# Performance work log

Measured on AMD Instinct MI355X. Metric: run time of the kernel, lower is better.

The kernel has to match this reference:

```python
import jax, jax.numpy as jnp
import numpy as np

N_POINTS = 200000   # number of voxels
N_CLUSTS = 4096     # number of clusters
P = 64              # points per cluster (regularized fixed size)
E = 32768           # number of (directed) edges


def setup_inputs() -> dict:
    key = jax.random.key(0)
    k1, k2, k3 = jax.random.split(key, 3)
    data = jax.random.normal(k1, (N_POINTS, 4), dtype=jnp.float32)
    clusts = jax.random.randint(k2, (N_CLUSTS, P), 0, N_POINTS, dtype=jnp.int64)
    edge_index = jax.random.randint(k3, (2, E), 0, N_CLUSTS, dtype=jnp.int64)
    return {"data": data, "clusts": clusts, "edge_index": edge_index}


def reference(data, clusts, edge_index):
    coords = data[:, 1:4]                      # [N, 3] voxel coordinates
    c1 = clusts[edge_index[0]]                 # [E, P] point indices of source cluster
    c2 = clusts[edge_index[1]]                 # [E, P] point indices of target cluster
    x1 = coords[c1]                            # [E, P, 3]
    x2 = coords[c2]                            # [E, P, 3]
    e, p = c1.shape
    # pairwise squared distances per edge: [E, P, P]
    d2 = jnp.sum((x1[:, :, None, :] - x2[:, None, :, :]) ** 2, axis=-1)
    imin = jnp.argmin(d2.reshape(e, p * p), axis=1)   # flat argmin of closest pair
    i1 = imin // p
    i2 = imin % p
    v1 = jnp.take_along_axis(x1, i1[:, None, None], axis=1)[:, 0, :]  # [E, 3]
    v2 = jnp.take_along_axis(x2, i2[:, None, None], axis=1)[:, 0, :]  # [E, 3]
    disp = v1 - v2                                                    # [E, 3]
    lend = jnp.linalg.norm(disp, axis=1, keepdims=True)               # [E, 1]
    safe = jnp.where(lend > 0, lend, jnp.ones_like(lend))
    disp = jnp.where(lend > 0, disp / safe, disp)                     # unit displacement
    B = (disp[:, :, None] * disp[:, None, :]).reshape(e, 9)           # outer product, flat
    return jnp.concatenate([v1, v2, disp, lend, B], axis=1)           # [E, 19]
```

## Files before the change

### kernel.cpp

```cpp
#include <hip/hip_runtime.h>

#ifndef FLT_MAX
#define FLT_MAX 3.402823466e+38f
#endif

typedef float v2f __attribute__((ext_vector_type(2)));
typedef float v4f __attribute__((ext_vector_type(4)));

__device__ __forceinline__ float sel3(int i, float a, float b, float c) {
    return i == 0 ? a : (i == 1 ? b : c);
}

__device__ __forceinline__ float sel4(int i, float a, float b, float c, float d) {
    return i == 0 ? a : (i == 1 ? b : (i == 2 ? c : d));
}

__device__ __forceinline__ float d2f(float ax, float ay, float az,
                                     float bx, float by, float bz) {
    const float dx = __fsub_rn(ax, bx);
    const float dy = __fsub_rn(ay, by);
    const float dz = __fsub_rn(az, bz);
    return __builtin_fmaf(dx, dx, __builtin_fmaf(dy, dy, __fmul_rn(dz, dz)));
}

__device__ __forceinline__ v2f d2p(v2f ax, v2f ay, v2f az, v2f bx, v2f by, v2f bz) {
    const v2f dx = ax - bx, dy = ay - by, dz = az - bz;
    return __builtin_elementwise_fma(dx, dx,
           __builtin_elementwise_fma(dy, dy, dz * dz));
}

#define SLICE 196

__global__ __launch_bounds__(256, 4) void clustgeo_edge_kernel(
    const float* __restrict__ data,
    const int*   __restrict__ clusts,
    const int*   __restrict__ eidx,
    float*       __restrict__ out,
    int E)
{
    const int wave = threadIdx.x >> 6;
    const int lane = threadIdx.x & 63;
    const int t    = lane & 15;
    const int gsh  = lane & 48;
    const int e    = blockIdx.x * 16 + wave * 4 + (lane >> 4);
    const int ec   = e < E ? e : (E - 1);

    __shared__ __align__(16) float sx[4][4][SLICE];

    const int ca = eidx[ec];
    const int cb = eidx[E + ec];

    const int4 P1 = *reinterpret_cast<const int4*>(clusts + ca * 64 + 4 * t);
    const int4 P2 = *reinterpret_cast<const int4*>(clusts + cb * 64 + 4 * t);
    const float4 q10 = *reinterpret_cast<const float4*>(data + (size_t)P1.x * 4);
    const float4 q11 = *reinterpret_cast<const float4*>(data + (size_t)P1.y * 4);
    const float4 q12 = *reinterpret_cast<const float4*>(data + (size_t)P1.z * 4);
    const float4 q13 = *reinterpret_cast<const float4*>(data + (size_t)P1.w * 4);
    const float4 q20 = *reinterpret_cast<const float4*>(data + (size_t)P2.x * 4);
    const float4 q21 = *reinterpret_cast<const float4*>(data + (size_t)P2.y * 4);
    const float4 q22 = *reinterpret_cast<const float4*>(data + (size_t)P2.z * 4);
    const float4 q23 = *reinterpret_cast<const float4*>(data + (size_t)P2.w * 4);
    const float r0x=q10.y, r0y=q10.z, r0z=q10.w;
    const float r1x=q11.y, r1y=q11.z, r1z=q11.w;
    const float r2x=q12.y, r2y=q12.z, r2z=q12.w;
    const float r3x=q13.y, r3y=q13.z, r3z=q13.w;
    const float c0x=q20.y, c0y=q20.z, c0z=q20.w;
    const float c1x=q21.y, c1y=q21.z, c1z=q21.w;
    const float c2x=q22.y, c2y=q22.z, c2z=q22.w;
    const float c3x=q23.y, c3y=q23.z, c3z=q23.w;

    float* slice = &sx[wave][lane >> 4][0];
    *reinterpret_cast<v4f*>(slice + 4 * t)       = (v4f){c0x, c1x, c2x, c3x};
    *reinterpret_cast<v4f*>(slice + 64 + 4 * t)  = (v4f){c0y, c1y, c2y, c3y};
    *reinterpret_cast<v4f*>(slice + 128 + 4 * t) = (v4f){c0z, c1z, c2z, c3z};

    const v4f* SL = reinterpret_cast<const v4f*>(slice);

    v2f a0 = {FLT_MAX, FLT_MAX}, a1 = {FLT_MAX, FLT_MAX};
    v2f a2 = {FLT_MAX, FLT_MAX}, a3 = {FLT_MAX, FLT_MAX};
    #pragma unroll 2
    for (int g = 0; g < 16; ++g) {
        const v4f X = SL[g];
        const v4f Y = SL[16 + g];
        const v4f Z = SL[32 + g];
        const v2f xlo = X.xy, xhi = X.zw, ylo = Y.xy, yhi = Y.zw, zlo = Z.xy, zhi = Z.zw;
        a0 = __builtin_elementwise_min(a0, d2p((v2f){r0x,r0x},(v2f){r0y,r0y},(v2f){r0z,r0z}, xlo, ylo, zlo));
        a0 = __builtin_elementwise_min(a0, d2p((v2f){r0x,r0x},(v2f){r0y,r0y},(v2f){r0z,r0z}, xhi, yhi, zhi));
        a1 = __builtin_elementwise_min(a1, d2p((v2f){r1x,r1x},(v2f){r1y,r1y},(v2f){r1z,r1z}, xlo, ylo, zlo));
        a1 = __builtin_elementwise_min(a1, d2p((v2f){r1x,r1x},(v2f){r1y,r1y},(v2f){r1z,r1z}, xhi, yhi, zhi));
        a2 = __builtin_elementwise_min(a2, d2p((v2f){r2x,r2x},(v2f){r2y,r2y},(v2f){r2z,r2z}, xlo, ylo, zlo));
        a2 = __builtin_elementwise_min(a2, d2p((v2f){r2x,r2x},(v2f){r2y,r2y},(v2f){r2z,r2z}, xhi, yhi, zhi));
        a3 = __builtin_elementwise_min(a3, d2p((v2f){r3x,r3x},(v2f){r3y,r3y},(v2f){r3z,r3z}, xlo, ylo, zlo));
        a3 = __builtin_elementwise_min(a3, d2p((v2f){r3x,r3x},(v2f){r3y,r3y},(v2f){r3z,r3z}, xhi, yhi, zhi));
    }
    const float m0 = fminf(a0.x, a0.y);
    const float m1 = fminf(a1.x, a1.y);
    const float m2 = fminf(a2.x, a2.y);
    const float m3 = fminf(a3.x, a3.y);

    float bmn = fminf(fminf(m0, m1), fminf(m2, m3));
    #pragma unroll
    for (int off = 8; off; off >>= 1) bmn = fminf(bmn, __shfl_xor(bmn, off, 64));

    const unsigned g0 = (unsigned)(__ballot(m0 == bmn) >> gsh) & 0xFFFFu;
    const unsigned g1 = (unsigned)(__ballot(m1 == bmn) >> gsh) & 0xFFFFu;
    const unsigned g2 = (unsigned)(__ballot(m2 == bmn) >> gsh) & 0xFFFFu;
    const unsigned g3 = (unsigned)(__ballot(m3 == bmn) >> gsh) & 0xFFFFu;
    const int t1 = __builtin_ctz(g0 | g1 | g2 | g3);
    const int s1 = (g0 >> t1) & 1 ? 0 : (g1 >> t1) & 1 ? 1 : (g2 >> t1) & 1 ? 2 : 3;

    const float v1x = __shfl(sel4(s1, r0x, r1x, r2x, r3x), gsh + t1, 64);
    const float v1y = __shfl(sel4(s1, r0y, r1y, r2y, r3y), gsh + t1, 64);
    const float v1z = __shfl(sel4(s1, r0z, r1z, r2z, r3z), gsh + t1, 64);

    const float d0 = d2f(v1x, v1y, v1z, c0x, c0y, c0z);
    const float d1 = d2f(v1x, v1y, v1z, c1x, c1y, c1z);
    const float d2_ = d2f(v1x, v1y, v1z, c2x, c2y, c2z);
    const float d3 = d2f(v1x, v1y, v1z, c3x, c3y, c3z);
    const unsigned h0 = (unsigned)(__ballot(d0 == bmn) >> gsh) & 0xFFFFu;
    const unsigned h1 = (unsigned)(__ballot(d1 == bmn) >> gsh) & 0xFFFFu;
    const unsigned h2 = (unsigned)(__ballot(d2_ == bmn) >> gsh) & 0xFFFFu;
    const unsigned h3 = (unsigned)(__ballot(d3 == bmn) >> gsh) & 0xFFFFu;
    const int t2 = __builtin_ctz(h0 | h1 | h2 | h3);
    const int s2 = (h0 >> t2) & 1 ? 0 : (h1 >> t2) & 1 ? 1 : (h2 >> t2) & 1 ? 2 : 3;

    const float v2x = __shfl(sel4(s2, c0x, c1x, c2x, c3x), gsh + t2, 64);
    const float v2y = __shfl(sel4(s2, c0y, c1y, c2y, c3y), gsh + t2, 64);
    const float v2z = __shfl(sel4(s2, c0z, c1z, c2z, c3z), gsh + t2, 64);

    float dx = v1x - v2x, dy = v1y - v2y, dz = v1z - v2z;
    const float lend = sqrtf(dx * dx + dy * dy + dz * dz);
    if (lend > 0.f) { dx /= lend; dy /= lend; dz /= lend; }

    if (e < E) {
        float* orow = out + (size_t)e * 19;
        float o;
        if (t < 3)       o = sel3(t,     v1x, v1y, v1z);
        else if (t < 6)  o = sel3(t - 3, v2x, v2y, v2z);
        else if (t < 9)  o = sel3(t - 6, dx, dy, dz);
        else if (t == 9) o = lend;
        else {
            const int k = t - 10;
            o = sel3(k / 3, dx, dy, dz) * sel3(k % 3, dx, dy, dz);
        }
        orow[t] = o;
        if (t < 3) {
            const int k = t + 6;
            orow[16 + t] = sel3(k / 3, dx, dy, dz) * sel3(k % 3, dx, dy, dz);
        }
    }
}

extern "C" void kernel_launch(void* const* d_in, const int* in_sizes, int n_in,
                              void* d_out, int out_size, void* d_ws, size_t ws_size,
                              hipStream_t stream) {
    const float* data   = (const float*)d_in[0];
    const int*   clusts = (const int*)d_in[1];
    const int*   eidx   = (const int*)d_in[2];
    float*       out    = (float*)d_out;
    const int E = in_sizes[2] / 2;
    const int blocks = (E + 15) / 16;
    clustgeo_edge_kernel<<<blocks, 256, 0, stream>>>(data, clusts, eidx, out, E);
}
```

Measured before the change: 31.87 us.

## Pre-gather cluster coordinates into SoA table before per-edge scan

Adds a pre-pass kernel that gathers each cluster's 64 point coordinates into a contiguous SoA table (x, y, z rows) in workspace. The per-edge kernel then reads coalesced float4 vectors from this table instead of doing a double indirection through clusts and scattered 16-byte loads from data for every edge. This avoids re-gathering the same cluster points about 16 times across edges, at the cost of an extra kernel launch and a round trip to the table (about 3 MB). If the workspace is too small, it falls back to the original single kernel.

Result: slower. 35.45 us (+11.2%).

```diff
diff --git a/kernel.cpp b/kernel.cpp
--- a/kernel.cpp
+++ b/kernel.cpp
@@ -29,11 +29,27 @@
            __builtin_elementwise_fma(dy, dy, dz * dz));
 }
 
-#define SLICE 196
-
-__global__ __launch_bounds__(256, 4) void clustgeo_edge_kernel(
+__global__ __launch_bounds__(256) void build_table_kernel(
     const float* __restrict__ data,
     const int*   __restrict__ clusts,
+    float*       __restrict__ T,
+    int C)
+{
+    const int c = blockIdx.x * 4 + (threadIdx.x >> 6);
+    const int p = threadIdx.x & 63;
+    if (c >= C) return;
+    const int pid = clusts[c * 64 + p];
+    const float4 d = *reinterpret_cast<const float4*>(data + (size_t)pid * 4);
+    float* row = T + (size_t)c * 192;
+    row[p]       = d.y;
+    row[p + 64]  = d.z;
+    row[p + 128] = d.w;
+}
+
+#define SLICE 196
+
+__global__ __launch_bounds__(256, 4) void clustgeo_scan_kernel(
+    const float* __restrict__ T,
     const int*   __restrict__ eidx,
     float*       __restrict__ out,
     int E)
@@ -49,30 +65,24 @@
 
     const int ca = eidx[ec];
     const int cb = eidx[E + ec];
-
-    const int4 P1 = *reinterpret_cast<const int4*>(clusts + ca * 64 + 4 * t);
-    const int4 P2 = *reinterpret_cast<const int4*>(clusts + cb * 64 + 4 * t);
-    const float4 q10 = *reinterpret_cast<const float4*>(data + (size_t)P1.x * 4);
-    const float4 q11 = *reinterpret_cast<const float4*>(data + (size_t)P1.y * 4);
-    const float4 q12 = *reinterpret_cast<const float4*>(data + (size_t)P1.z * 4);
-    const float4 q13 = *reinterpret_cast<const float4*>(data + (size_t)P1.w * 4);
-    const float4 q20 = *reinterpret_cast<const float4*>(data + (size_t)P2.x * 4);
-    const float4 q21 = *reinterpret_cast<const float4*>(data + (size_t)P2.y * 4);
-    const float4 q22 = *reinterpret_cast<const float4*>(data + (size_t)P2.z * 4);
-    const float4 q23 = *reinterpret_cast<const float4*>(data + (size_t)P2.w * 4);
-    const float r0x=q10.y, r0y=q10.z, r0z=q10.w;
-    const float r1x=q11.y, r1y=q11.z, r1z=q11.w;
-    const float r2x=q12.y, r2y=q12.z, r2z=q12.w;
-    const float r3x=q13.y, r3y=q13.z, r3z=q13.w;
-    const float c0x=q20.y, c0y=q20.z, c0z=q20.w;
-    const float c1x=q21.y, c1y=q21.z, c1z=q21.w;
-    const float c2x=q22.y, c2y=q22.z, c2z=q22.w;
-    const float c3x=q23.y, c3y=q23.z, c3z=q23.w;
+    const float* Ta = T + (size_t)ca * 192;
+    const float* Tb = T + (size_t)cb * 192;
+
+    const v4f RX = *reinterpret_cast<const v4f*>(Ta + 4 * t);
+    const v4f RY = *reinterpret_cast<const v4f*>(Ta + 64 + 4 * t);
+    const v4f RZ = *reinterpret_cast<const v4f*>(Ta + 128 + 4 * t);
+    const v4f CX = *reinterpret_cast<const v4f*>(Tb + 4 * t);
+    const v4f CY = *reinterpret_cast<const v4f*>(Tb + 64 + 4 * t);
+    const v4f CZ = *reinterpret_cast<const v4f*>(Tb + 128 + 4 * t);
 
     float* slice = &sx[wave][lane >> 4][0];
-    *reinterpret_cast<v4f*>(slice + 4 * t)       = (v4f){c0x, c1x, c2x, c3x};
-    *reinterpret_cast<v4f*>(slice + 64 + 4 * t)  = (v4f){c0y, c1y, c2y, c3y};
-    *reinterpret_cast<v4f*>(slice + 128 + 4 * t) = (v4f){c0z, c1z, c2z, c3z};
+    *reinterpret_cast<v4f*>(slice + 4 * t)       = CX;
+    *reinterpret_cast<v4f*>(slice + 64 + 4 * t)  = CY;
+    *reinterpret_cast<v4f*>(slice + 128 + 4 * t) = CZ;
+
+    const float r0x=RX.x, r1x=RX.y, r2x=RX.z, r3x=RX.w;
+    const float r0y=RY.x, r1y=RY.y, r2y=RY.z, r3y=RY.w;
+    const float r0z=RZ.x, r1z=RZ.y, r2z=RZ.z, r3z=RZ.w;
 
     const v4f* SL = reinterpret_cast<const v4f*>(slice);
 
@@ -109,14 +119,14 @@
     const int t1 = __builtin_ctz(g0 | g1 | g2 | g3);
     const int s1 = (g0 >> t1) & 1 ? 0 : (g1 >> t1) & 1 ? 1 : (g2 >> t1) & 1 ? 2 : 3;
 
-    const float v1x = __shfl(sel4(s1, r0x, r1x, r2x, r3x), gsh + t1, 64);
-    const float v1y = __shfl(sel4(s1, r0y, r1y, r2y, r3y), gsh + t1, 64);
-    const float v1z = __shfl(sel4(s1, r0z, r1z, r2z, r3z), gsh + t1, 64);
-
-    const float d0 = d2f(v1x, v1y, v1z, c0x, c0y, c0z);
-    const float d1 = d2f(v1x, v1y, v1z, c1x, c1y, c1z);
-    const float d2_ = d2f(v1x, v1y, v1z, c2x, c2y, c2z);
-    const float d3 = d2f(v1x, v1y, v1z, c3x, c3y, c3z);
+    const float v1x = __shfl(sel4(s1, RX.x, RX.y, RX.z, RX.w), gsh + t1, 64);
+    const float v1y = __shfl(sel4(s1, RY.x, RY.y, RY.z, RY.w), gsh + t1, 64);
+    const float v1z = __shfl(sel4(s1, RZ.x, RZ.y, RZ.z, RZ.w), gsh + t1, 64);
+
+    const float d0 = d2f(v1x, v1y, v1z, CX.x, CY.x, CZ.x);
+    const float d1 = d2f(v1x, v1y, v1z, CX.y, CY.y, CZ.y);
+    const float d2_ = d2f(v1x, v1y, v1z, CX.z, CY.z, CZ.z);
+    const float d3 = d2f(v1x, v1y, v1z, CX.w, CY.w, CZ.w);
     const unsigned h0 = (unsigned)(__ballot(d0 == bmn) >> gsh) & 0xFFFFu;
     const unsigned h1 = (unsigned)(__ballot(d1 == bmn) >> gsh) & 0xFFFFu;
     const unsigned h2 = (unsigned)(__ballot(d2_ == bmn) >> gsh) & 0xFFFFu;
@@ -124,9 +134,9 @@
     const int t2 = __builtin_ctz(h0 | h1 | h2 | h3);
     const int s2 = (h0 >> t2) & 1 ? 0 : (h1 >> t2) & 1 ? 1 : (h2 >> t2) & 1 ? 2 : 3;
 
-    const float v2x = __shfl(sel4(s2, c0x, c1x, c2x, c3x), gsh + t2, 64);
-    const float v2y = __shfl(sel4(s2, c0y, c1y, c2y, c3y), gsh + t2, 64);
-    const float v2z = __shfl(sel4(s2, c0z, c1z, c2z, c3z), gsh + t2, 64);
+    const float v2x = __shfl(sel4(s2, CX.x, CX.y, CX.z, CX.w), gsh + t2, 64);
+    const float v2y = __shfl(sel4(s2, CY.x, CY.y, CY.z, CY.w), gsh + t2, 64);
+    const float v2z = __shfl(sel4(s2, CZ.x, CZ.y, CZ.z, CZ.w), gsh + t2, 64);
 
     float dx = v1x - v2x, dy = v1y - v2y, dz = v1z - v2z;
     const float lend = sqrtf(dx * dx + dy * dy + dz * dz);
@@ -151,6 +161,115 @@
     }
 }
 
+__global__ __launch_bounds__(256, 4) void clustgeo_edge_fallback(
+    const float* __restrict__ data,
+    const int*   __restrict__ clusts,
+    const int*   __restrict__ eidx,
+    float*       __restrict__ out,
+    int E)
+{
+    const int wave = threadIdx.x >> 6;
+    const int lane = threadIdx.x & 63;
+    const int t    = lane & 15;
+    const int gsh  = lane & 48;
+    const int e    = blockIdx.x * 16 + wave * 4 + (lane >> 4);
+    const int ec   = e < E ? e : (E - 1);
+
+    __shared__ __align__(16) float sx[4][4][SLICE];
+
+    const int ca = eidx[ec];
+    const int cb = eidx[E + ec];
+    const int4 P1 = *reinterpret_cast<const int4*>(clusts + ca * 64 + 4 * t);
+    const int4 P2 = *reinterpret_cast<const int4*>(clusts + cb * 64 + 4 * t);
+    const float4 q10 = *reinterpret_cast<const float4*>(data + (size_t)P1.x * 4);
+    const float4 q11 = *reinterpret_cast<const float4*>(data + (size_t)P1.y * 4);
+    const float4 q12 = *reinterpret_cast<const float4*>(data + (size_t)P1.z * 4);
+    const float4 q13 = *reinterpret_cast<const float4*>(data + (size_t)P1.w * 4);
+    const float4 q20 = *reinterpret_cast<const float4*>(data + (size_t)P2.x * 4);
+    const float4 q21 = *reinterpret_cast<const float4*>(data + (size_t)P2.y * 4);
+    const float4 q22 = *reinterpret_cast<const float4*>(data + (size_t)P2.z * 4);
+    const float4 q23 = *reinterpret_cast<const float4*>(data + (size_t)P2.w * 4);
+    const v4f RX = {q10.y, q11.y, q12.y, q13.y};
+    const v4f RY = {q10.z, q11.z, q12.z, q13.z};
+    const v4f RZ = {q10.w, q11.w, q12.w, q13.w};
+    const v4f CX = {q20.y, q21.y, q22.y, q23.y};
+    const v4f CY = {q20.z, q21.z, q22.z, q23.z};
+    const v4f CZ = {q20.w, q21.w, q22.w, q23.w};
+
+    float* slice = &sx[wave][lane >> 4][0];
+    *reinterpret_cast<v4f*>(slice + 4 * t)       = CX;
+    *reinterpret_cast<v4f*>(slice + 64 + 4 * t)  = CY;
+    *reinterpret_cast<v4f*>(slice + 128 + 4 * t) = CZ;
+
+    const v4f* SL = reinterpret_cast<const v4f*>(slice);
+    v2f a0 = {FLT_MAX, FLT_MAX}, a1 = {FLT_MAX, FLT_MAX};
+    v2f a2 = {FLT_MAX, FLT_MAX}, a3 = {FLT_MAX, FLT_MAX};
+    #pragma unroll 2
+    for (int g = 0; g < 16; ++g) {
+        const v4f X = SL[g];
+        const v4f Y = SL[16 + g];
+        const v4f Z = SL[32 + g];
+        const v2f xlo = X.xy, xhi = X.zw, ylo = Y.xy, yhi = Y.zw, zlo = Z.xy, zhi = Z.zw;
+        a0 = __builtin_elementwise_min(a0, d2p((v2f){RX.x,RX.x},(v2f){RY.x,RY.x},(v2f){RZ.x,RZ.x}, xlo, ylo, zlo));
+        a0 = __builtin_elementwise_min(a0, d2p((v2f){RX.x,RX.x},(v2f){RY.x,RY.x},(v2f){RZ.x,RZ.x}, xhi, yhi, zhi));
+        a1 = __builtin_elementwise_min(a1, d2p((v2f){RX.y,RX.y},(v2f){RY.y,RY.y},(v2f){RZ.y,RZ.y}, xlo, ylo, zlo));
+        a1 = __builtin_elementwise_min(a1, d2p((v2f){RX.y,RX.y},(v2f){RY.y,RY.y},(v2f){RZ.y,RZ.y}, xhi, yhi, zhi));
+        a2 = __builtin_elementwise_min(a2, d2p((v2f){RX.z,RX.z},(v2f){RY.z,RY.z},(v2f){RZ.z,RZ.z}, xlo, ylo, zlo));
+        a2 = __builtin_elementwise_min(a2, d2p((v2f){RX.z,RX.z},(v2f){RY.z,RY.z},(v2f){RZ.z,RZ.z}, xhi, yhi, zhi));
+        a3 = __builtin_elementwise_min(a3, d2p((v2f){RX.w,RX.w},(v2f){RY.w,RY.w},(v2f){RZ.w,RZ.w}, xlo, ylo, zlo));
+        a3 = __builtin_elementwise_min(a3, d2p((v2f){RX.w,RX.w},(v2f){RY.w,RY.w},(v2f){RZ.w,RZ.w}, xhi, yhi, zhi));
+    }
+    const float m0 = fminf(a0.x, a0.y);
+    const float m1 = fminf(a1.x, a1.y);
+    const float m2 = fminf(a2.x, a2.y);
+    const float m3 = fminf(a3.x, a3.y);
+    float bmn = fminf(fminf(m0, m1), fminf(m2, m3));
+    #pragma unroll
+    for (int off = 8; off; off >>= 1) bmn = fminf(bmn, __shfl_xor(bmn, off, 64));
+    const unsigned g0 = (unsigned)(__ballot(m0 == bmn) >> gsh) & 0xFFFFu;
+    const unsigned g1 = (unsigned)(__ballot(m1 == bmn) >> gsh) & 0xFFFFu;
+    const unsigned g2 = (unsigned)(__ballot(m2 == bmn) >> gsh) & 0xFFFFu;
+    const unsigned g3 = (unsigned)(__ballot(m3 == bmn) >> gsh) & 0xFFFFu;
+    const int t1 = __builtin_ctz(g0 | g1 | g2 | g3);
+    const int s1 = (g0 >> t1) & 1 ? 0 : (g1 >> t1) & 1 ? 1 : (g2 >> t1) & 1 ? 2 : 3;
+    const float v1x = __shfl(sel4(s1, RX.x, RX.y, RX.z, RX.w), gsh + t1, 64);
+    const float v1y = __shfl(sel4(s1, RY.x, RY.y, RY.z, RY.w), gsh + t1, 64);
+    const float v1z = __shfl(sel4(s1, RZ.x, RZ.y, RZ.z, RZ.w), gsh + t1, 64);
+    const float d0 = d2f(v1x, v1y, v1z, CX.x, CY.x, CZ.x);
+    const float d1 = d2f(v1x, v1y, v1z, CX.y, CY.y, CZ.y);
+    const float d2_ = d2f(v1x, v1y, v1z, CX.z, CY.z, CZ.z);
+    const float d3 = d2f(v1x, v1y, v1z, CX.w, CY.w, CZ.w);
+    const unsigned h0 = (unsigned)(__ballot(d0 == bmn) >> gsh) & 0xFFFFu;
+    const unsigned h1 = (unsigned)(__ballot(d1 == bmn) >> gsh) & 0xFFFFu;
+    const unsigned h2 = (unsigned)(__ballot(d2_ == bmn) >> gsh) & 0xFFFFu;
+    const unsigned h3 = (unsigned)(__ballot(d3 == bmn) >> gsh) & 0xFFFFu;
+    const int t2 = __builtin_ctz(h0 | h1 | h2 | h3);
+    const int s2 = (h0 >> t2) & 1 ? 0 : (h1 >> t2) & 1 ? 1 : (h2 >> t2) & 1 ? 2 : 3;
+    const float v2x = __shfl(sel4(s2, CX.x, CX.y, CX.z, CX.w), gsh + t2, 64);
+    const float v2y = __shfl(sel4(s2, CY.x, CY.y, CY.z, CY.w), gsh + t2, 64);
+    const float v2z = __shfl(sel4(s2, CZ.x, CZ.y, CZ.z, CZ.w), gsh + t2, 64);
+    float dx = v1x - v2x, dy = v1y - v2y, dz = v1z - v2z;
+    const float lend = sqrtf(dx * dx + dy * dy + dz * dz);
+    if (lend > 0.f) { dx /= lend; dy /= lend; dz /= lend; }
+    if (e < E) {
+        float* orow = out + (size_t)e * 19;
+        float o;
+        if (t < 3)       o = sel3(t,     v1x, v1y, v1z);
+        else if (t < 6)  o = sel3(t - 3, v2x, v2y, v2z);
+        else if (t < 9)  o = sel3(t - 6, dx, dy, dz);
+        else if (t == 9) o = lend;
+        else {
+            const int k = t - 10;
+            o = sel3(k / 3, dx, dy, dz) * sel3(k % 3, dx, dy, dz);
+        }
+        orow[t] = o;
+        if (t < 3) {
+            const int k = t + 6;
+            orow[16 + t] = sel3(k / 3, dx, dy, dz) * sel3(k % 3, dx, dy, dz);
+        }
+    }
+}
+
 extern "C" void kernel_launch(void* const* d_in, const int* in_sizes, int n_in,
                               void* d_out, int out_size, void* d_ws, size_t ws_size,
                               hipStream_t stream) {
@@ -159,6 +278,14 @@
     const int*   eidx   = (const int*)d_in[2];
     float*       out    = (float*)d_out;
     const int E = in_sizes[2] / 2;
-    const int blocks = (E + 15) / 16;
-    clustgeo_edge_kernel<<<blocks, 256, 0, stream>>>(data, clusts, eidx, out, E);
-}
+    const int C = in_sizes[1] / 64;
+    const size_t tbytes = (size_t)C * 192 * sizeof(float);
+
+    if (ws_size >= tbytes) {
+        float* T = (float*)d_ws;
+        build_table_kernel<<<(C + 3) / 4, 256, 0, stream>>>(data, clusts, T, C);
+        clustgeo_scan_kernel<<<(E + 15) / 16, 256, 0, stream>>>(T, eidx, out, E);
+    } else {
+        clustgeo_edge_fallback<<<(E + 15) / 16, 256, 0, stream>>>(data, clusts, eidx, out, E);
+    }
+}
```

## Filter closest-pair candidates with packed fp16 distances, refine rows exactly in fp32

Applied to the files above, without the earlier changes.

The 64x64 pairwise distance scan now runs in packed fp16 (v_pk_add/fma/min via inline asm) on negated, fp16-packed target coordinates held in LDS, with half the LDS footprint. Rows whose fp16 minimum falls within an error bound of the best are kept as candidates. Each candidate row is then recomputed exactly in fp32, one row at a time across the 16-lane group, to recover the true argmin. This halves the work of the main loop but adds a serial refinement loop whose trip count depends on the data, and it relies on a heuristic error bound that could miss the true minimum or overflow fp16 for large coordinates.

Result: slower. 60.75 us (+90.6%).

```diff
diff --git a/kernel.cpp b/kernel.cpp
--- a/kernel.cpp
+++ b/kernel.cpp
@@ -4,34 +4,50 @@
 #define FLT_MAX 3.402823466e+38f
 #endif
 
-typedef float v2f __attribute__((ext_vector_type(2)));
-typedef float v4f __attribute__((ext_vector_type(4)));
-
 __device__ __forceinline__ float sel3(int i, float a, float b, float c) {
     return i == 0 ? a : (i == 1 ? b : c);
 }
-
 __device__ __forceinline__ float sel4(int i, float a, float b, float c, float d) {
     return i == 0 ? a : (i == 1 ? b : (i == 2 ? c : d));
 }
 
-__device__ __forceinline__ float d2f(float ax, float ay, float az,
-                                     float bx, float by, float bz) {
+__device__ __forceinline__ float d2np(float ax, float ay, float az,
+                                      float bx, float by, float bz) {
     const float dx = __fsub_rn(ax, bx);
     const float dy = __fsub_rn(ay, by);
     const float dz = __fsub_rn(az, bz);
-    return __builtin_fmaf(dx, dx, __builtin_fmaf(dy, dy, __fmul_rn(dz, dz)));
-}
-
-__device__ __forceinline__ v2f d2p(v2f ax, v2f ay, v2f az, v2f bx, v2f by, v2f bz) {
-    const v2f dx = ax - bx, dy = ay - by, dz = az - bz;
-    return __builtin_elementwise_fma(dx, dx,
-           __builtin_elementwise_fma(dy, dy, dz * dz));
-}
-
-#define SLICE 196
-
-__global__ __launch_bounds__(256, 4) void clustgeo_edge_kernel(
+    return __fadd_rn(__fadd_rn(__fmul_rn(dx, dx), __fmul_rn(dy, dy)),
+                     __fmul_rn(dz, dz));
+}
+
+__device__ __forceinline__ unsigned pk2(float a, float b) {
+    unsigned short ua = __builtin_bit_cast(unsigned short, (_Float16)a);
+    unsigned short ub = __builtin_bit_cast(unsigned short, (_Float16)b);
+    return (unsigned)ua | ((unsigned)ub << 16);
+}
+__device__ __forceinline__ float lo16f(unsigned u) {
+    return (float)__builtin_bit_cast(_Float16, (unsigned short)(u & 0xFFFFu));
+}
+__device__ __forceinline__ float hi16f(unsigned u) {
+    return (float)__builtin_bit_cast(_Float16, (unsigned short)(u >> 16));
+}
+
+__device__ __forceinline__ void f16step(unsigned& acc, unsigned rx, unsigned ry,
+                                        unsigned rz, unsigned ncx, unsigned ncy,
+                                        unsigned ncz) {
+    unsigned dx, dy, dz;
+    asm("v_pk_add_f16 %0, %4, %7\n\t"
+        "v_pk_add_f16 %1, %5, %8\n\t"
+        "v_pk_add_f16 %2, %6, %9\n\t"
+        "v_pk_mul_f16 %2, %2, %2\n\t"
+        "v_pk_fma_f16 %2, %1, %1, %2\n\t"
+        "v_pk_fma_f16 %2, %0, %0, %2\n\t"
+        "v_pk_min_f16 %3, %3, %2"
+        : "=&v"(dx), "=&v"(dy), "=&v"(dz), "+v"(acc)
+        : "v"(rx), "v"(ry), "v"(rz), "v"(ncx), "v"(ncy), "v"(ncz));
+}
+
+__global__ __launch_bounds__(256, 4) void clustgeo_f16filter(
     const float* __restrict__ data,
     const int*   __restrict__ clusts,
     const int*   __restrict__ eidx,
@@ -45,11 +61,10 @@
     const int e    = blockIdx.x * 16 + wave * 4 + (lane >> 4);
     const int ec   = e < E ? e : (E - 1);
 
-    __shared__ __align__(16) float sx[4][4][SLICE];
+    __shared__ __align__(16) unsigned sx[4][4][112];
 
     const int ca = eidx[ec];
     const int cb = eidx[E + ec];
-
     const int4 P1 = *reinterpret_cast<const int4*>(clusts + ca * 64 + 4 * t);
     const int4 P2 = *reinterpret_cast<const int4*>(clusts + cb * 64 + 4 * t);
     const float4 q10 = *reinterpret_cast<const float4*>(data + (size_t)P1.x * 4);
@@ -69,68 +84,121 @@
     const float c2x=q22.y, c2y=q22.z, c2z=q22.w;
     const float c3x=q23.y, c3y=q23.z, c3z=q23.w;
 
-    float* slice = &sx[wave][lane >> 4][0];
-    *reinterpret_cast<v4f*>(slice + 4 * t)       = (v4f){c0x, c1x, c2x, c3x};
-    *reinterpret_cast<v4f*>(slice + 64 + 4 * t)  = (v4f){c0y, c1y, c2y, c3y};
-    *reinterpret_cast<v4f*>(slice + 128 + 4 * t) = (v4f){c0z, c1z, c2z, c3z};
-
-    const v4f* SL = reinterpret_cast<const v4f*>(slice);
-
-    v2f a0 = {FLT_MAX, FLT_MAX}, a1 = {FLT_MAX, FLT_MAX};
-    v2f a2 = {FLT_MAX, FLT_MAX}, a3 = {FLT_MAX, FLT_MAX};
+    unsigned* slice = &sx[wave][lane >> 4][0];
+    slice[2*t]        = pk2(-c0x, -c1x);  slice[2*t + 1]      = pk2(-c2x, -c3x);
+    slice[32 + 2*t]   = pk2(-c0y, -c1y);  slice[32 + 2*t + 1] = pk2(-c2y, -c3y);
+    slice[64 + 2*t]   = pk2(-c0z, -c1z);  slice[64 + 2*t + 1] = pk2(-c2z, -c3z);
+
+    const unsigned rr0x = pk2(r0x, r0x), rr0y = pk2(r0y, r0y), rr0z = pk2(r0z, r0z);
+    const unsigned rr1x = pk2(r1x, r1x), rr1y = pk2(r1y, r1y), rr1z = pk2(r1z, r1z);
+    const unsigned rr2x = pk2(r2x, r2x), rr2y = pk2(r2y, r2y), rr2z = pk2(r2z, r2z);
+    const unsigned rr3x = pk2(r3x, r3x), rr3y = pk2(r3y, r3y), rr3z = pk2(r3z, r3z);
+
+    const uint4* SU = reinterpret_cast<const uint4*>(slice);
+    unsigned a0 = 0x7C007C00u, a1 = 0x7C007C00u;
+    unsigned a2 = 0x7C007C00u, a3 = 0x7C007C00u;
+
     #pragma unroll 2
-    for (int g = 0; g < 16; ++g) {
-        const v4f X = SL[g];
-        const v4f Y = SL[16 + g];
-        const v4f Z = SL[32 + g];
-        const v2f xlo = X.xy, xhi = X.zw, ylo = Y.xy, yhi = Y.zw, zlo = Z.xy, zhi = Z.zw;
-        a0 = __builtin_elementwise_min(a0, d2p((v2f){r0x,r0x},(v2f){r0y,r0y},(v2f){r0z,r0z}, xlo, ylo, zlo));
-        a0 = __builtin_elementwise_min(a0, d2p((v2f){r0x,r0x},(v2f){r0y,r0y},(v2f){r0z,r0z}, xhi, yhi, zhi));
-        a1 = __builtin_elementwise_min(a1, d2p((v2f){r1x,r1x},(v2f){r1y,r1y},(v2f){r1z,r1z}, xlo, ylo, zlo));
-        a1 = __builtin_elementwise_min(a1, d2p((v2f){r1x,r1x},(v2f){r1y,r1y},(v2f){r1z,r1z}, xhi, yhi, zhi));
-        a2 = __builtin_elementwise_min(a2, d2p((v2f){r2x,r2x},(v2f){r2y,r2y},(v2f){r2z,r2z}, xlo, ylo, zlo));
-        a2 = __builtin_elementwise_min(a2, d2p((v2f){r2x,r2x},(v2f){r2y,r2y},(v2f){r2z,r2z}, xhi, yhi, zhi));
-        a3 = __builtin_elementwise_min(a3, d2p((v2f){r3x,r3x},(v2f){r3y,r3y},(v2f){r3z,r3z}, xlo, ylo, zlo));
-        a3 = __builtin_elementwise_min(a3, d2p((v2f){r3x,r3x},(v2f){r3y,r3y},(v2f){r3z,r3z}, xhi, yhi, zhi));
-    }
-    const float m0 = fminf(a0.x, a0.y);
-    const float m1 = fminf(a1.x, a1.y);
-    const float m2 = fminf(a2.x, a2.y);
-    const float m3 = fminf(a3.x, a3.y);
-
-    float bmn = fminf(fminf(m0, m1), fminf(m2, m3));
+    for (int g = 0; g < 8; ++g) {
+        const uint4 X = SU[g];
+        const uint4 Y = SU[8 + g];
+        const uint4 Z = SU[16 + g];
+        f16step(a0, rr0x, rr0y, rr0z, X.x, Y.x, Z.x);
+        f16step(a0, rr0x, rr0y, rr0z, X.y, Y.y, Z.y);
+        f16step(a0, rr0x, rr0y, rr0z, X.z, Y.z, Z.z);
+        f16step(a0, rr0x, rr0y, rr0z, X.w, Y.w, Z.w);
+        f16step(a1, rr1x, rr1y, rr1z, X.x, Y.x, Z.x);
+        f16step(a1, rr1x, rr1y, rr1z, X.y, Y.y, Z.y);
+        f16step(a1, rr1x, rr1y, rr1z, X.z, Y.z, Z.z);
+        f16step(a1, rr1x, rr1y, rr1z, X.w, Y.w, Z.w);
+        f16step(a2, rr2x, rr2y, rr2z, X.x, Y.x, Z.x);
+        f16step(a2, rr2x, rr2y, rr2z, X.y, Y.y, Z.y);
+        f16step(a2, rr2x, rr2y, rr2z, X.z, Y.z, Z.z);
+        f16step(a2, rr2x, rr2y, rr2z, X.w, Y.w, Z.w);
+        f16step(a3, rr3x, rr3y, rr3z, X.x, Y.x, Z.x);
+        f16step(a3, rr3x, rr3y, rr3z, X.y, Y.y, Z.y);
+        f16step(a3, rr3x, rr3y, rr3z, X.z, Y.z, Z.z);
+        f16step(a3, rr3x, rr3y, rr3z, X.w, Y.w, Z.w);
+    }
+
+    const float rm0 = fminf(lo16f(a0), hi16f(a0));
+    const float rm1 = fminf(lo16f(a1), hi16f(a1));
+    const float rm2 = fminf(lo16f(a2), hi16f(a2));
+    const float rm3 = fminf(lo16f(a3), hi16f(a3));
+
+    float bm = fminf(fminf(rm0, rm1), fminf(rm2, rm3));
     #pragma unroll
-    for (int off = 8; off; off >>= 1) bmn = fminf(bmn, __shfl_xor(bmn, off, 64));
-
-    const unsigned g0 = (unsigned)(__ballot(m0 == bmn) >> gsh) & 0xFFFFu;
-    const unsigned g1 = (unsigned)(__ballot(m1 == bmn) >> gsh) & 0xFFFFu;
-    const unsigned g2 = (unsigned)(__ballot(m2 == bmn) >> gsh) & 0xFFFFu;
-    const unsigned g3 = (unsigned)(__ballot(m3 == bmn) >> gsh) & 0xFFFFu;
-    const int t1 = __builtin_ctz(g0 | g1 | g2 | g3);
-    const int s1 = (g0 >> t1) & 1 ? 0 : (g1 >> t1) & 1 ? 1 : (g2 >> t1) & 1 ? 2 : 3;
-
+    for (int off = 8; off; off >>= 1) bm = fminf(bm, __shfl_xor(bm, off, 64));
+
+    float Ml = fmaxf(fmaxf(fmaxf(fabsf(r0x), fabsf(r0y)), fmaxf(fabsf(r0z), fabsf(r1x))),
+               fmaxf(fmaxf(fabsf(r1y), fabsf(r1z)), fmaxf(fabsf(r2x), fabsf(r2y))));
+    Ml = fmaxf(Ml, fmaxf(fmaxf(fabsf(r2z), fabsf(r3x)), fmaxf(fabsf(r3y), fabsf(r3z))));
+    Ml = fmaxf(Ml, fmaxf(fmaxf(fabsf(c0x), fabsf(c0y)), fmaxf(fabsf(c0z), fabsf(c1x))));
+    Ml = fmaxf(Ml, fmaxf(fmaxf(fabsf(c1y), fabsf(c1z)), fmaxf(fabsf(c2x), fabsf(c2y))));
+    Ml = fmaxf(Ml, fmaxf(fmaxf(fabsf(c2z), fabsf(c3x)), fmaxf(fabsf(c3y), fabsf(c3z))));
+    #pragma unroll
+    for (int off = 8; off; off >>= 1) Ml = fmaxf(Ml, __shfl_xor(Ml, off, 64));
+
+    const float eps = 0.006f * (Ml * sqrtf(bm) + bm) + 1e-3f;
+    const float T = bm + 2.0f * eps;
+
+    int fb = (rm0 <= T ? 1 : 0) | (rm1 <= T ? 2 : 0) |
+             (rm2 <= T ? 4 : 0) | (rm3 <= T ? 8 : 0);
+
+    float bestVal = FLT_MAX;
+    int bestRow = 0, bestCol = 0;
+    while (true) {
+        int rl = fb ? (4 * t + __builtin_ctz((unsigned)fb)) : 999;
+        int rstar = rl;
+        #pragma unroll
+        for (int off = 8; off; off >>= 1) {
+            const int o = __shfl_xor(rstar, off, 64);
+            rstar = o < rstar ? o : rstar;
+        }
+        if (!__ballot(rstar != 999)) break;
+        if (rstar != 999) {
+            if (rl == rstar) fb &= fb - 1;
+            const int ss = rstar & 3, tt = rstar >> 2;
+            const float vx = __shfl(sel4(ss, r0x, r1x, r2x, r3x), gsh + tt, 64);
+            const float vy = __shfl(sel4(ss, r0y, r1y, r2y, r3y), gsh + tt, 64);
+            const float vz = __shfl(sel4(ss, r0z, r1z, r2z, r3z), gsh + tt, 64);
+            const float e0 = d2np(vx, vy, vz, c0x, c0y, c0z);
+            const float e1 = d2np(vx, vy, vz, c1x, c1y, c1z);
+            const float e2 = d2np(vx, vy, vz, c2x, c2y, c2z);
+            const float e3 = d2np(vx, vy, vz, c3x, c3y, c3z);
+            float rmn = fminf(fminf(e0, e1), fminf(e2, e3));
+            #pragma unroll
+            for (int off = 8; off; off >>= 1) rmn = fminf(rmn, __shfl_xor(rmn, off, 64));
+            if (rmn < bestVal) {
+                bestVal = rmn;
+                bestRow = rstar;
+                const unsigned h0 = (unsigned)(__ballot(e0 == rmn) >> gsh) & 0xFFFFu;
+                const unsigned h1 = (unsigned)(__ballot(e1 == rmn) >> gsh) & 0xFFFFu;
+                const unsigned h2 = (unsigned)(__ballot(e2 == rmn) >> gsh) & 0xFFFFu;
+                const unsigned h3 = (unsigned)(__ballot(e3 == rmn) >> gsh) & 0xFFFFu;
+                const int t2i = __builtin_ctz(h0 | h1 | h2 | h3);
+                const int s2 = (h0 >> t2i) & 1 ? 0 : (h1 >> t2i) & 1 ? 1
+                             : (h2 >> t2i) & 1 ? 2 : 3;
+                bestCol = 4 * t2i + s2;
+            }
+        }
+    }
+
+    const int s1 = bestRow & 3, t1 = bestRow >> 2;
     const float v1x = __shfl(sel4(s1, r0x, r1x, r2x, r3x), gsh + t1, 64);
     const float v1y = __shfl(sel4(s1, r0y, r1y, r2y, r3y), gsh + t1, 64);
     const float v1z = __shfl(sel4(s1, r0z, r1z, r2z, r3z), gsh + t1, 64);
-
-    const float d0 = d2f(v1x, v1y, v1z, c0x, c0y, c0z);
-    const float d1 = d2f(v1x, v1y, v1z, c1x, c1y, c1z);
-    const float d2_ = d2f(v1x, v1y, v1z, c2x, c2y, c2z);
-    const float d3 = d2f(v1x, v1y, v1z, c3x, c3y, c3z);
-    const unsigned h0 = (unsigned)(__ballot(d0 == bmn) >> gsh) & 0xFFFFu;
-    const unsigned h1 = (unsigned)(__ballot(d1 == bmn) >> gsh) & 0xFFFFu;
-    const unsigned h2 = (unsigned)(__ballot(d2_ == bmn) >> gsh) & 0xFFFFu;
-    const unsigned h3 = (unsigned)(__ballot(d3 == bmn) >> gsh) & 0xFFFFu;
-    const int t2 = __builtin_ctz(h0 | h1 | h2 | h3);
-    const int s2 = (h0 >> t2) & 1 ? 0 : (h1 >> t2) & 1 ? 1 : (h2 >> t2) & 1 ? 2 : 3;
-
-    const float v2x = __shfl(sel4(s2, c0x, c1x, c2x, c3x), gsh + t2, 64);
-    const float v2y = __shfl(sel4(s2, c0y, c1y, c2y, c3y), gsh + t2, 64);
-    const float v2z = __shfl(sel4(s2, c0z, c1z, c2z, c3z), gsh + t2, 64);
+    const int s2c = bestCol & 3, t2c = bestCol >> 2;
+    const float v2x = __shfl(sel4(s2c, c0x, c1x, c2x, c3x), gsh + t2c, 64);
+    const float v2y = __shfl(sel4(s2c, c0y, c1y, c2y, c3y), gsh + t2c, 64);
+    const float v2z = __shfl(sel4(s2c, c0z, c1z, c2z, c3z), gsh + t2c, 64);
 
     float dx = v1x - v2x, dy = v1y - v2y, dz = v1z - v2z;
     const float lend = sqrtf(dx * dx + dy * dy + dz * dz);
-    if (lend > 0.f) { dx /= lend; dy /= lend; dz /= lend; }
+    if (lend > 0.f) {
+        const float inv = 1.0f / lend;
+        dx *= inv; dy *= inv; dz *= inv;
+    }
 
     if (e < E) {
         float* orow = out + (size_t)e * 19;
@@ -160,5 +228,5 @@
     float*       out    = (float*)d_out;
     const int E = in_sizes[2] / 2;
     const int blocks = (E + 15) / 16;
-    clustgeo_edge_kernel<<<blocks, 256, 0, stream>>>(data, clusts, eidx, out, E);
-}
+    clustgeo_f16filter<<<blocks, 256, 0, stream>>>(data, clusts, eidx, out, E);
+}
```
